# Optimization experiments

Measured on AMD Instinct MI355X. Metric: run time of the kernel, lower is better.

Reference implementation:

```python
import jax, jax.numpy as jnp
import numpy as np

FG_FRACTION = 0.25
FG_THRESH = 0.5
BG_HI = 0.5
BG_LO = 0.1
BATCHSIZE = 256
FG_ROIS_PER_IMAGE = int(round(FG_FRACTION * BATCHSIZE))  # 64


def _iou(a, b):
    # a: [N,4], b: [K,4]; keras_rcnn overlap uses the +1 pixel convention
    ax1, ay1, ax2, ay2 = a[:, 0:1], a[:, 1:2], a[:, 2:3], a[:, 3:4]
    bx1, by1, bx2, by2 = b[:, 0], b[:, 1], b[:, 2], b[:, 3]
    iw = jnp.maximum(jnp.minimum(ax2, bx2) - jnp.maximum(ax1, bx1) + 1.0, 0.0)
    ih = jnp.maximum(jnp.minimum(ay2, by2) - jnp.maximum(ay1, by1) + 1.0, 0.0)
    inter = iw * ih  # [N,K]
    area_a = (ax2 - ax1 + 1.0) * (ay2 - ay1 + 1.0)  # [N,1]
    area_b = (bx2 - bx1 + 1.0) * (by2 - by1 + 1.0)  # [K]
    return inter / (area_a + area_b - inter)


def _bbox_transform(ex, gt):
    ew = ex[:, 2] - ex[:, 0] + 1.0
    eh = ex[:, 3] - ex[:, 1] + 1.0
    ecx = ex[:, 0] + 0.5 * ew
    ecy = ex[:, 1] + 0.5 * eh
    gw = gt[:, 2] - gt[:, 0] + 1.0
    gh = gt[:, 3] - gt[:, 1] + 1.0
    gcx = gt[:, 0] + 0.5 * gw
    gcy = gt[:, 1] + 0.5 * gh
    tx = (gcx - ecx) / ew
    ty = (gcy - ecy) / eh
    tw = jnp.log(gw / ew)
    th = jnp.log(gh / eh)
    return jnp.stack([tx, ty, tw, th], axis=1)


def _random_boxes(key, n, img=1000.0):
    k1, k2, k3, k4 = jax.random.split(key, 4)
    cx = jax.random.uniform(k1, (n,)) * (img - 200.0) + 100.0
    cy = jax.random.uniform(k2, (n,)) * (img - 200.0) + 100.0
    w = jax.random.uniform(k3, (n,)) * 150.0 + 30.0
    h = jax.random.uniform(k4, (n,)) * 150.0 + 30.0
    return jnp.stack([cx - 0.5 * w, cy - 0.5 * h, cx + 0.5 * w, cy + 0.5 * h], axis=1)


def setup_inputs() -> dict:
    key = jax.random.key(0)
    N, K, C = 50000, 500, 81
    kg, kl, kj, kr = jax.random.split(key, 4)
    gt = _random_boxes(kg, K)
    labels_int = jax.random.randint(kl, (K,), 1, C)
    gt_labels = jax.nn.one_hot(labels_int, C, dtype=jnp.float32)
    # 10*K jittered copies of gt boxes -> guaranteed fg pool; rest random -> bg pool
    reps = 10
    fg_props = jnp.tile(gt, (reps, 1)) + jax.random.normal(kj, (reps * K, 4)) * 3.0
    rand_props = _random_boxes(kr, N - reps * K)
    proposals = jnp.concatenate([fg_props, rand_props], axis=0)[None]  # [1,N,4]
    return {"proposals": proposals, "gt_labels": gt_labels[None], "gt_boxes": gt[None]}


def _proposal_target(proposals, gt_labels, gt_boxes):
    p = proposals[0]
    g = gt_boxes[0].astype(jnp.float32)
    lab1h = gt_labels[0]
    num_classes = lab1h.shape[1]

    all_rois = jnp.concatenate([p, g], axis=0)  # [N+K,4]
    n_total = all_rois.shape[0]

    gt_cls = jnp.argmax(lab1h, axis=1)                 # [K]
    overlaps = _iou(all_rois, g)                       # [N+K,K]
    gt_assignment = jnp.argmax(overlaps, axis=1)       # [N+K]
    max_overlaps = jnp.max(overlaps, axis=1)           # [N+K]
    labels_all = gt_cls[gt_assignment]                 # [N+K]

    fg_mask = max_overlaps >= FG_THRESH
    bg_mask = (max_overlaps < BG_HI) & (max_overlaps >= BG_LO)

    order = jnp.arange(n_total)
    # stable: fg/bg indices first (in index order), others pushed to the back
    fg_sorted = jnp.argsort(jnp.where(fg_mask, order, order + n_total))
    bg_sorted = jnp.argsort(jnp.where(bg_mask, order, order + n_total))

    n_fg = jnp.sum(fg_mask)
    n_bg = jnp.sum(bg_mask)
    fg_count = jnp.minimum(FG_ROIS_PER_IMAGE, n_fg)
    bg_count = jnp.minimum(BATCHSIZE - fg_count, n_bg)

    slots = jnp.arange(BATCHSIZE)
    is_fg_slot = slots < fg_count
    keep = jnp.where(
        is_fg_slot,
        fg_sorted[jnp.clip(slots, 0, n_total - 1)],
        bg_sorted[jnp.clip(slots - fg_count, 0, n_total - 1)],
    )
    valid = slots < (fg_count + bg_count)

    rois = all_rois[keep]                                   # [256,4]
    labels_kept = jnp.where(is_fg_slot & valid, labels_all[keep], 0)  # bg -> 0
    gt_kept = g[gt_assignment[keep]]                        # [256,4]

    targets = _bbox_transform(rois, gt_kept)                # [256,4]
    oh = jax.nn.one_hot(labels_kept, num_classes, dtype=jnp.float32)
    pos = (labels_kept > 0).astype(jnp.float32)
    # expand to 4K form: only the assigned class gets nonzero targets
    bbox_targets = (oh * pos[:, None])[:, :, None] * targets[:, None, :]
    bbox_targets = bbox_targets.reshape(BATCHSIZE, 4 * num_classes)

    labels_out = oh  # one_hot of (fg labels, 0 for bg)
    return rois[None], labels_out[None], bbox_targets[None]


def reference(proposals, gt_labels, gt_boxes):
    return _proposal_target(proposals, gt_labels, gt_boxes)
```

## Files before the change

kernel.cpp:

```cpp
#include <hip/hip_runtime.h>

#define BATCH   256
#define FG_CAP  64
#define BG_CAP  192
#define NB_CAP  256
#define M_ROIS  2
#define GRP     8
#define ROIS_PB (32 * M_ROIS)

__global__ __launch_bounds__(256) void pt_classify(
    const float* __restrict__ props, const float* __restrict__ gtb,
    const float* __restrict__ gtl,
    int* __restrict__ packed, int* __restrict__ gtcls,
    int n_prop, int K, int C, int n_total, int roi_blocks)
{
    if ((int)blockIdx.x >= roi_blocks) {
        int t = ((int)blockIdx.x - roi_blocks) * 256 + (int)threadIdx.x;
        if (t < K) {
            const float* row = gtl + (size_t)t * C;
            float best = row[0]; int bc = 0;
            for (int c = 1; c < C; ++c) {
                float v = row[c];
                if (v > best) { best = v; bc = c; }
            }
            gtcls[t] = bc;
        }
        return;
    }

    __shared__ float4 s_gt[512];
    for (int k = threadIdx.x; k < K; k += 256)
        s_gt[k] = ((const float4*)gtb)[k];
    __syncthreads();

    const int grp   = (int)threadIdx.x >> 3;
    const int slice = (int)threadIdx.x & (GRP - 1);

    float4 a[M_ROIS]; float area_a[M_ROIS]; int ri[M_ROIS]; bool live[M_ROIS];
    #pragma unroll
    for (int m = 0; m < M_ROIS; ++m) {
        int i = (int)blockIdx.x * ROIS_PB + m * 32 + grp;
        ri[m] = i; live[m] = (i < n_total);
        if (live[m]) {
            a[m] = (i < n_prop) ? ((const float4*)props)[i]
                                : ((const float4*)gtb)[i - n_prop];
        } else {
            a[m] = make_float4(0.f, 0.f, 0.f, 0.f);
        }
        area_a[m] = __fmul_rn(__fadd_rn(__fsub_rn(a[m].z, a[m].x), 1.0f),
                              __fadd_rn(__fsub_rn(a[m].w, a[m].y), 1.0f));
    }

    float bi[M_ROIS], bd[M_ROIS]; int bk[M_ROIS];
    #pragma unroll
    for (int m = 0; m < M_ROIS; ++m) { bi[m] = -1.0f; bd[m] = 1.0f; bk[m] = 0x7FFFFFFF; }

    #pragma unroll 4
    for (int k = slice; k < K; k += GRP) {
        float4 g = s_gt[k];
        float area_g = __fmul_rn(__fadd_rn(__fsub_rn(g.z, g.x), 1.0f),
                                 __fadd_rn(__fsub_rn(g.w, g.y), 1.0f));
        #pragma unroll
        for (int m = 0; m < M_ROIS; ++m) {
            float iw = fmaxf(__fadd_rn(__fsub_rn(fminf(a[m].z, g.z), fmaxf(a[m].x, g.x)), 1.0f), 0.0f);
            float ih = fmaxf(__fadd_rn(__fsub_rn(fminf(a[m].w, g.w), fmaxf(a[m].y, g.y)), 1.0f), 0.0f);
            float inter = __fmul_rn(iw, ih);
            float denom = __fsub_rn(__fadd_rn(area_a[m], area_g), inter);
            if (inter * bd[m] > bi[m] * denom) { bi[m] = inter; bd[m] = denom; bk[m] = k; }
        }
    }

    #pragma unroll
    for (int mask = 1; mask < GRP; mask <<= 1) {
        #pragma unroll
        for (int m = 0; m < M_ROIS; ++m) {
            float oi = __shfl_xor(bi[m], mask, 64);
            float od = __shfl_xor(bd[m], mask, 64);
            int   ok = __shfl_xor(bk[m], mask, 64);
            float lhs = oi * bd[m], rhs = bi[m] * od;
            if (lhs > rhs || (lhs == rhs && ok < bk[m])) { bi[m] = oi; bd[m] = od; bk[m] = ok; }
        }
    }

    if (slice == 0) {
        #pragma unroll
        for (int m = 0; m < M_ROIS; ++m) {
            if (live[m]) {
                float iou = __fdiv_rn(bi[m], bd[m]);
                int cls = 0;
                if (iou >= 0.5f)      cls = 1;
                else if (iou >= 0.1f) cls = 2;
                packed[ri[m]] = bk[m] | (cls << 16);
            }
        }
    }
}

__global__ __launch_bounds__(1024) void pt_compact(
    const int* __restrict__ packed,
    int* __restrict__ fg_list, int* __restrict__ bg_list,
    int* __restrict__ nb_list, int* __restrict__ counts, int n_total)
{
    __shared__ int w_f[16], w_b[16], w_n[16];
    __shared__ int s_run[3], s_stop;
    const int tid = (int)threadIdx.x;
    if (tid == 0) { s_run[0] = 0; s_run[1] = 0; s_run[2] = 0; s_stop = 0; }
    __syncthreads();

    const int lane = tid & 63, wave = tid >> 6;
    const unsigned long long ltm = (1ull << lane) - 1ull;

    for (int base = 0; base < n_total; base += 8192) {
        int idx0 = base + tid * 8;
        int code = 0;
        if (idx0 + 7 < n_total) {
            int4 p0 = ((const int4*)packed)[idx0 >> 2];
            int4 p1 = ((const int4*)packed)[(idx0 >> 2) + 1];
            code  = (p0.x >> 16)        | ((p0.y >> 16) << 2)
                  | ((p0.z >> 16) << 4) | ((p0.w >> 16) << 6)
                  | ((p1.x >> 16) << 8) | ((p1.y >> 16) << 10)
                  | ((p1.z >> 16) << 12)| ((p1.w >> 16) << 14);
        } else {
            #pragma unroll
            for (int j = 0; j < 8; ++j) {
                int c = (idx0 + j < n_total) ? (packed[idx0 + j] >> 16) : 3;
                code |= c << (2 * j);
            }
        }

        int eF = 0, eB = 0, eN = 0, tF = 0, tB = 0, tN = 0;
        #pragma unroll
        for (int j = 0; j < 8; ++j) {
            int c = (code >> (2 * j)) & 3;
            unsigned long long bF = __ballot(c == 1);
            unsigned long long bB = __ballot(c == 2);
            unsigned long long bN = __ballot(c == 0 || c == 1);
            eF += (int)__popcll(bF & ltm); tF += (int)__popcll(bF);
            eB += (int)__popcll(bB & ltm); tB += (int)__popcll(bB);
            eN += (int)__popcll(bN & ltm); tN += (int)__popcll(bN);
        }
        if (lane == 0) { w_f[wave] = tF; w_b[wave] = tB; w_n[wave] = tN; }
        int r0 = s_run[0], r1 = s_run[1], r2 = s_run[2];
        __syncthreads();

        int pf = 0, pb = 0, pn = 0;
        for (int w = 0; w < wave; ++w) { pf += w_f[w]; pb += w_b[w]; pn += w_n[w]; }
        int rF = r0 + pf + eF, rB = r1 + pb + eB, rN = r2 + pn + eN;
        #pragma unroll
        for (int j = 0; j < 8; ++j) {
            int c = (code >> (2 * j)) & 3;
            int idx = idx0 + j;
            if (c == 1)           { if (rF < FG_CAP) fg_list[rF] = idx; rF++; }
            if (c == 2)           { if (rB < BG_CAP) bg_list[rB] = idx; rB++; }
            if (c == 0 || c == 1) { if (rN < NB_CAP) nb_list[rN] = idx; rN++; }
        }
        if (tid == 0) {
            int sf = 0, sb = 0, sn = 0;
            for (int w = 0; w < 16; ++w) { sf += w_f[w]; sb += w_b[w]; sn += w_n[w]; }
            s_run[0] += sf; s_run[1] += sb; s_run[2] += sn;
            if (s_run[0] >= FG_CAP && s_run[1] >= BG_CAP) s_stop = 1;
        }
        __syncthreads();
        if (s_stop) break;
    }
    if (tid == 0) { counts[0] = s_run[0]; counts[1] = s_run[1]; counts[2] = s_run[2]; }
}

__global__ __launch_bounds__(128) void pt_output(
    const float* __restrict__ props, const float* __restrict__ gtb,
    const int* __restrict__ packed, const int* __restrict__ gtcls,
    const int* __restrict__ fg_list, const int* __restrict__ bg_list,
    const int* __restrict__ nb_list, const int* __restrict__ counts,
    float* __restrict__ out, int n_prop, int K, int C)
{
    __shared__ float sh[8];
    __shared__ int   sh_label;
    int s = blockIdx.x;

    if (threadIdx.x == 0) {
        int fg_total = counts[0], bg_total = counts[1];
        int fg_count = min(FG_CAP, fg_total);
        bool is_fg = (s < fg_count);
        int keep;
        if (is_fg) keep = fg_list[s];
        else { int j = s - fg_count; keep = (j < bg_total) ? bg_list[j] : nb_list[j - bg_total]; }
        int pk = packed[keep];
        int assign = pk & 0xFFFF;
        int label = is_fg ? gtcls[assign] : 0;

        float4 roi = (keep < n_prop) ? ((const float4*)props)[keep]
                                     : ((const float4*)gtb)[keep - n_prop];
        float4 g = ((const float4*)gtb)[assign];

        float ew  = roi.z - roi.x + 1.0f;
        float eh  = roi.w - roi.y + 1.0f;
        float ecx = roi.x + 0.5f * ew;
        float ecy = roi.y + 0.5f * eh;
        float gw  = g.z - g.x + 1.0f;
        float gh  = g.w - g.y + 1.0f;
        float gcx = g.x + 0.5f * gw;
        float gcy = g.y + 0.5f * gh;
        sh[0] = roi.x; sh[1] = roi.y; sh[2] = roi.z; sh[3] = roi.w;
        sh[4] = (gcx - ecx) / ew;
        sh[5] = (gcy - ecy) / eh;
        sh[6] = logf(gw / ew);
        sh[7] = logf(gh / eh);
        sh_label = label;
    }
    __syncthreads();

    int label = sh_label;

    if (threadIdx.x < 4) out[s * 4 + threadIdx.x] = sh[threadIdx.x];

    float* outl = out + 4 * BATCH;
    for (int c = threadIdx.x; c < C; c += 128)
        outl[s * C + c] = (c == label) ? 1.0f : 0.0f;

    float4* outb = (float4*)(out + 4 * BATCH + (size_t)BATCH * C) + (size_t)s * C;
    float4 tv = make_float4(sh[4], sh[5], sh[6], sh[7]);
    float4 zv = make_float4(0.f, 0.f, 0.f, 0.f);
    for (int c = threadIdx.x; c < C; c += 128)
        outb[c] = (label > 0 && c == label) ? tv : zv;
}

extern "C" void kernel_launch(void* const* d_in, const int* in_sizes, int n_in,
                              void* d_out, int out_size, void* d_ws, size_t ws_size,
                              hipStream_t stream)
{
    const float* props = (const float*)d_in[0];
    const float* gtl   = (const float*)d_in[1];
    const float* gtb   = (const float*)d_in[2];
    float* out = (float*)d_out;

    int n_prop  = in_sizes[0] / 4;
    int K       = in_sizes[2] / 4;
    int C       = in_sizes[1] / K;
    int n_total = n_prop + K;

    int* ws_packed = (int*)d_ws;
    int* ws_gtcls  = ws_packed + ((n_total + 3) & ~3);
    int* ws_fg     = ws_gtcls + ((K + 3) & ~3);
    int* ws_bg     = ws_fg + FG_CAP;
    int* ws_nb     = ws_bg + BG_CAP;
    int* ws_cnt    = ws_nb + NB_CAP;

    int roi_blocks = (n_total + ROIS_PB - 1) / ROIS_PB;
    int gt_blocks  = (K + 255) / 256;

    pt_classify<<<roi_blocks + gt_blocks, 256, 0, stream>>>(
        props, gtb, gtl, ws_packed, ws_gtcls, n_prop, K, C, n_total, roi_blocks);
    pt_compact<<<1, 1024, 0, stream>>>(
        ws_packed, ws_fg, ws_bg, ws_nb, ws_cnt, n_total);
    pt_output<<<BATCH, 128, 0, stream>>>(
        props, gtb, ws_packed, ws_gtcls, ws_fg, ws_bg, ws_nb, ws_cnt,
        out, n_prop, K, C);
}
```

Baseline: 85.72 us.

## Fuse compaction and output kernels with spin-wait handoff via keep array

After: 87.48 us. 1.02x slower.

```diff
diff --git a/kernel.cpp b/kernel.cpp
--- a/kernel.cpp
+++ b/kernel.cpp
@@ -7,15 +7,18 @@
 #define M_ROIS  2
 #define GRP     8
 #define ROIS_PB (32 * M_ROIS)
+#define KV_SENTINEL (-1)
 
 __global__ __launch_bounds__(256) void pt_classify(
     const float* __restrict__ props, const float* __restrict__ gtb,
     const float* __restrict__ gtl,
     int* __restrict__ packed, int* __restrict__ gtcls,
+    int* __restrict__ keep_arr,
     int n_prop, int K, int C, int n_total, int roi_blocks)
 {
     if ((int)blockIdx.x >= roi_blocks) {
         int t = ((int)blockIdx.x - roi_blocks) * 256 + (int)threadIdx.x;
+        if (t < BATCH) keep_arr[t] = KV_SENTINEL;
         if (t < K) {
             const float* row = gtl + (size_t)t * C;
             float best = row[0]; int bc = 0;
@@ -96,132 +99,135 @@
     }
 }
 
-__global__ __launch_bounds__(1024) void pt_compact(
-    const int* __restrict__ packed,
-    int* __restrict__ fg_list, int* __restrict__ bg_list,
-    int* __restrict__ nb_list, int* __restrict__ counts, int n_total)
-{
-    __shared__ int w_f[16], w_b[16], w_n[16];
-    __shared__ int s_run[3], s_stop;
-    const int tid = (int)threadIdx.x;
-    if (tid == 0) { s_run[0] = 0; s_run[1] = 0; s_run[2] = 0; s_stop = 0; }
-    __syncthreads();
-
-    const int lane = tid & 63, wave = tid >> 6;
-    const unsigned long long ltm = (1ull << lane) - 1ull;
-
-    for (int base = 0; base < n_total; base += 8192) {
-        int idx0 = base + tid * 8;
-        int code = 0;
-        if (idx0 + 7 < n_total) {
-            int4 p0 = ((const int4*)packed)[idx0 >> 2];
-            int4 p1 = ((const int4*)packed)[(idx0 >> 2) + 1];
-            code  = (p0.x >> 16)        | ((p0.y >> 16) << 2)
-                  | ((p0.z >> 16) << 4) | ((p0.w >> 16) << 6)
-                  | ((p1.x >> 16) << 8) | ((p1.y >> 16) << 10)
-                  | ((p1.z >> 16) << 12)| ((p1.w >> 16) << 14);
-        } else {
-            #pragma unroll
-            for (int j = 0; j < 8; ++j) {
-                int c = (idx0 + j < n_total) ? (packed[idx0 + j] >> 16) : 3;
-                code |= c << (2 * j);
-            }
-        }
-
-        int eF = 0, eB = 0, eN = 0, tF = 0, tB = 0, tN = 0;
-        #pragma unroll
-        for (int j = 0; j < 8; ++j) {
-            int c = (code >> (2 * j)) & 3;
-            unsigned long long bF = __ballot(c == 1);
-            unsigned long long bB = __ballot(c == 2);
-            unsigned long long bN = __ballot(c == 0 || c == 1);
-            eF += (int)__popcll(bF & ltm); tF += (int)__popcll(bF);
-            eB += (int)__popcll(bB & ltm); tB += (int)__popcll(bB);
-            eN += (int)__popcll(bN & ltm); tN += (int)__popcll(bN);
-        }
-        if (lane == 0) { w_f[wave] = tF; w_b[wave] = tB; w_n[wave] = tN; }
-        int r0 = s_run[0], r1 = s_run[1], r2 = s_run[2];
-        __syncthreads();
-
-        int pf = 0, pb = 0, pn = 0;
-        for (int w = 0; w < wave; ++w) { pf += w_f[w]; pb += w_b[w]; pn += w_n[w]; }
-        int rF = r0 + pf + eF, rB = r1 + pb + eB, rN = r2 + pn + eN;
-        #pragma unroll
-        for (int j = 0; j < 8; ++j) {
-            int c = (code >> (2 * j)) & 3;
-            int idx = idx0 + j;
-            if (c == 1)           { if (rF < FG_CAP) fg_list[rF] = idx; rF++; }
-            if (c == 2)           { if (rB < BG_CAP) bg_list[rB] = idx; rB++; }
-            if (c == 0 || c == 1) { if (rN < NB_CAP) nb_list[rN] = idx; rN++; }
-        }
-        if (tid == 0) {
-            int sf = 0, sb = 0, sn = 0;
-            for (int w = 0; w < 16; ++w) { sf += w_f[w]; sb += w_b[w]; sn += w_n[w]; }
-            s_run[0] += sf; s_run[1] += sb; s_run[2] += sn;
-            if (s_run[0] >= FG_CAP && s_run[1] >= BG_CAP) s_stop = 1;
-        }
-        __syncthreads();
-        if (s_stop) break;
-    }
-    if (tid == 0) { counts[0] = s_run[0]; counts[1] = s_run[1]; counts[2] = s_run[2]; }
-}
-
-__global__ __launch_bounds__(128) void pt_output(
+__global__ __launch_bounds__(256) void pt_select_out(
     const float* __restrict__ props, const float* __restrict__ gtb,
     const int* __restrict__ packed, const int* __restrict__ gtcls,
-    const int* __restrict__ fg_list, const int* __restrict__ bg_list,
-    const int* __restrict__ nb_list, const int* __restrict__ counts,
-    float* __restrict__ out, int n_prop, int K, int C)
+    int* __restrict__ keep_arr,
+    float* __restrict__ out, int n_prop, int K, int C, int n_total)
 {
-    __shared__ float sh[8];
-    __shared__ int   sh_label;
-    int s = blockIdx.x;
-
-    if (threadIdx.x == 0) {
-        int fg_total = counts[0], bg_total = counts[1];
-        int fg_count = min(FG_CAP, fg_total);
+    const int tid = (int)threadIdx.x;
+
+    if (blockIdx.x == 0) {
+        __shared__ int l_fg[FG_CAP], l_bg[BG_CAP], l_nb[NB_CAP];
+        __shared__ int w_f[4], w_b[4], w_n[4];
+        __shared__ int s_run[3], s_stop;
+        if (tid == 0) { s_run[0] = 0; s_run[1] = 0; s_run[2] = 0; s_stop = 0; }
+        __syncthreads();
+
+        const int lane = tid & 63, wave = tid >> 6;
+        const unsigned long long ltm = (1ull << lane) - 1ull;
+
+        for (int base = 0; base < n_total; base += 4096) {
+            int idx0 = base + tid * 16;
+            unsigned int code = 0;
+            if (idx0 + 15 < n_total) {
+                #pragma unroll
+                for (int q = 0; q < 4; ++q) {
+                    int4 p = ((const int4*)packed)[(idx0 >> 2) + q];
+                    code |= (unsigned int)((p.x >> 16) & 3) << (8*q + 0);
+                    code |= (unsigned int)((p.y >> 16) & 3) << (8*q + 2);
+                    code |= (unsigned int)((p.z >> 16) & 3) << (8*q + 4);
+                    code |= (unsigned int)((p.w >> 16) & 3) << (8*q + 6);
+                }
+            } else {
+                #pragma unroll
+                for (int j = 0; j < 16; ++j) {
+                    unsigned int c = (idx0 + j < n_total) ? (unsigned int)((packed[idx0 + j] >> 16) & 3) : 3u;
+                    code |= c << (2 * j);
+                }
+            }
+
+            int eF = 0, eB = 0, eN = 0, tF = 0, tB = 0, tN = 0;
+            #pragma unroll
+            for (int j = 0; j < 16; ++j) {
+                unsigned int c = (code >> (2 * j)) & 3u;
+                unsigned long long bF = __ballot(c == 1u);
+                unsigned long long bB = __ballot(c == 2u);
+                unsigned long long bN = __ballot(c <= 1u);
+                eF += (int)__popcll(bF & ltm); tF += (int)__popcll(bF);
+                eB += (int)__popcll(bB & ltm); tB += (int)__popcll(bB);
+                eN += (int)__popcll(bN & ltm); tN += (int)__popcll(bN);
+            }
+            if (lane == 0) { w_f[wave] = tF; w_b[wave] = tB; w_n[wave] = tN; }
+            int r0 = s_run[0], r1 = s_run[1], r2 = s_run[2];
+            __syncthreads();
+
+            int pf = 0, pb = 0, pn = 0;
+            for (int w = 0; w < wave; ++w) { pf += w_f[w]; pb += w_b[w]; pn += w_n[w]; }
+            int rF = r0 + pf + eF, rB = r1 + pb + eB, rN = r2 + pn + eN;
+            #pragma unroll
+            for (int j = 0; j < 16; ++j) {
+                unsigned int c = (code >> (2 * j)) & 3u;
+                int idx = idx0 + j;
+                if (c == 1u) { if (rF < FG_CAP) l_fg[rF] = idx; rF++; }
+                if (c == 2u) { if (rB < BG_CAP) l_bg[rB] = idx; rB++; }
+                if (c <= 1u) { if (rN < NB_CAP) l_nb[rN] = idx; rN++; }
+            }
+            if (tid == 0) {
+                s_run[0] += w_f[0] + w_f[1] + w_f[2] + w_f[3];
+                s_run[1] += w_b[0] + w_b[1] + w_b[2] + w_b[3];
+                s_run[2] += w_n[0] + w_n[1] + w_n[2] + w_n[3];
+                if (s_run[0] >= FG_CAP && s_run[1] >= BG_CAP) s_stop = 1;
+            }
+            __syncthreads();
+            if (s_stop) break;
+        }
+
+        int fgt = s_run[0], bgt = s_run[1];
+        int fg_count = min(FG_CAP, fgt);
+        int s = tid;
         bool is_fg = (s < fg_count);
         int keep;
-        if (is_fg) keep = fg_list[s];
-        else { int j = s - fg_count; keep = (j < bg_total) ? bg_list[j] : nb_list[j - bg_total]; }
-        int pk = packed[keep];
-        int assign = pk & 0xFFFF;
-        int label = is_fg ? gtcls[assign] : 0;
-
-        float4 roi = (keep < n_prop) ? ((const float4*)props)[keep]
-                                     : ((const float4*)gtb)[keep - n_prop];
-        float4 g = ((const float4*)gtb)[assign];
-
-        float ew  = roi.z - roi.x + 1.0f;
-        float eh  = roi.w - roi.y + 1.0f;
-        float ecx = roi.x + 0.5f * ew;
-        float ecy = roi.y + 0.5f * eh;
-        float gw  = g.z - g.x + 1.0f;
-        float gh  = g.w - g.y + 1.0f;
-        float gcx = g.x + 0.5f * gw;
-        float gcy = g.y + 0.5f * gh;
-        sh[0] = roi.x; sh[1] = roi.y; sh[2] = roi.z; sh[3] = roi.w;
-        sh[4] = (gcx - ecx) / ew;
-        sh[5] = (gcy - ecy) / eh;
-        sh[6] = logf(gw / ew);
-        sh[7] = logf(gh / eh);
-        sh_label = label;
+        if (is_fg) keep = l_fg[s];
+        else { int j = s - fg_count; keep = (j < bgt) ? l_bg[j] : l_nb[j - bgt]; }
+        atomicExch(&keep_arr[s], keep | (is_fg ? (1 << 30) : 0));
+        return;
+    }
+
+    int s = (int)blockIdx.x - 1;
+    __shared__ int sh_kv;
+    if (tid == 0) {
+        int kv = atomicAdd(&keep_arr[s], 0);
+        while (kv == KV_SENTINEL) {
+            __builtin_amdgcn_s_sleep(8);
+            kv = atomicAdd(&keep_arr[s], 0);
+        }
+        sh_kv = kv;
     }
     __syncthreads();
 
-    int label = sh_label;
-
-    if (threadIdx.x < 4) out[s * 4 + threadIdx.x] = sh[threadIdx.x];
-
-    float* outl = out + 4 * BATCH;
-    for (int c = threadIdx.x; c < C; c += 128)
-        outl[s * C + c] = (c == label) ? 1.0f : 0.0f;
-
-    float4* outb = (float4*)(out + 4 * BATCH + (size_t)BATCH * C) + (size_t)s * C;
-    float4 tv = make_float4(sh[4], sh[5], sh[6], sh[7]);
+    int kv = sh_kv;
+    bool is_fg = (kv >> 30) & 1;
+    int keep = kv & 0x3FFFFFFF;
+
+    int assign = packed[keep] & 0xFFFF;
+    int label = is_fg ? gtcls[assign] : 0;
+
+    float4 roi = (keep < n_prop) ? ((const float4*)props)[keep]
+                                 : ((const float4*)gtb)[keep - n_prop];
+    float4 g = ((const float4*)gtb)[assign];
+
+    float ew  = roi.z - roi.x + 1.0f;
+    float eh  = roi.w - roi.y + 1.0f;
+    float ecx = roi.x + 0.5f * ew;
+    float ecy = roi.y + 0.5f * eh;
+    float gw  = g.z - g.x + 1.0f;
+    float gh  = g.w - g.y + 1.0f;
+    float gcx = g.x + 0.5f * gw;
+    float gcy = g.y + 0.5f * gh;
+    float4 tv = make_float4((gcx - ecx) / ew, (gcy - ecy) / eh,
+                            logf(gw / ew), logf(gh / eh));
     float4 zv = make_float4(0.f, 0.f, 0.f, 0.f);
-    for (int c = threadIdx.x; c < C; c += 128)
-        outb[c] = (label > 0 && c == label) ? tv : zv;
+
+    if (tid == 0) ((float4*)out)[s] = roi;
+
+    if (tid < C)
+        out[4 * BATCH + (size_t)s * C + tid] = (tid == label) ? 1.0f : 0.0f;
+
+    if (tid < C) {
+        float4* outb = (float4*)(out + 4 * BATCH + (size_t)BATCH * C) + (size_t)s * C;
+        outb[tid] = (label > 0 && tid == label) ? tv : zv;
+    }
 }
 
 extern "C" void kernel_launch(void* const* d_in, const int* in_sizes, int n_in,
@@ -240,19 +246,15 @@
 
     int* ws_packed = (int*)d_ws;
     int* ws_gtcls  = ws_packed + ((n_total + 3) & ~3);
-    int* ws_fg     = ws_gtcls + ((K + 3) & ~3);
-    int* ws_bg     = ws_fg + FG_CAP;
-    int* ws_nb     = ws_bg + BG_CAP;
-    int* ws_cnt    = ws_nb + NB_CAP;
+    int* ws_keep   = ws_gtcls + ((K + 3) & ~3);
 
     int roi_blocks = (n_total + ROIS_PB - 1) / ROIS_PB;
     int gt_blocks  = (K + 255) / 256;
 
     pt_classify<<<roi_blocks + gt_blocks, 256, 0, stream>>>(
-        props, gtb, gtl, ws_packed, ws_gtcls, n_prop, K, C, n_total, roi_blocks);
-    pt_compact<<<1, 1024, 0, stream>>>(
-        ws_packed, ws_fg, ws_bg, ws_nb, ws_cnt, n_total);
-    pt_output<<<BATCH, 128, 0, stream>>>(
-        props, gtb, ws_packed, ws_gtcls, ws_fg, ws_bg, ws_nb, ws_cnt,
-        out, n_prop, K, C);
+        props, gtb, gtl, ws_packed, ws_gtcls, ws_keep,
+        n_prop, K, C, n_total, roi_blocks);
+    pt_select_out<<<1 + BATCH, 256, 0, stream>>>(
+        props, gtb, ws_packed, ws_gtcls, ws_keep,
+        out, n_prop, K, C, n_total);
 }
```
